# Performance work log

Measured on AMD Instinct MI355X. Metric: run time of the kernel, lower is better.

The kernel has to match this reference:

```python
import jax, jax.numpy as jnp
import numpy as np

N_NODES = 100000
N_EDGES = 3200000
IN_CH = 32
HID = 16


def setup_inputs() -> dict:
    key = jax.random.key(0)
    ks = jax.random.split(key, 8)
    x = jax.random.normal(ks[0], (N_NODES, IN_CH), dtype=jnp.float32)
    edge_index = jax.random.randint(ks[1], (2, N_EDGES), 0, N_NODES, dtype=jnp.int64)
    s1 = 1.0 / np.sqrt(IN_CH)
    s2 = 1.0 / np.sqrt(HID)
    Wl1 = jax.random.normal(ks[2], (HID, IN_CH), dtype=jnp.float32) * s1
    Wr1 = jax.random.normal(ks[3], (HID, IN_CH), dtype=jnp.float32) * s1
    b1 = jnp.zeros((HID,), dtype=jnp.float32)
    Wl2 = jax.random.normal(ks[4], (1, HID), dtype=jnp.float32) * s2
    Wr2 = jax.random.normal(ks[5], (1, HID), dtype=jnp.float32) * s2
    b2 = jnp.zeros((1,), dtype=jnp.float32)
    return {"x": x, "edge_index": edge_index, "Wl1": Wl1, "Wr1": Wr1,
            "b1": b1, "Wl2": Wl2, "Wr2": Wr2, "b2": b2}


def _sage_conv(h, src, dst, deg_inv, Wl, Wr, b):
    # mean aggregation of source features at destination nodes
    msg_sum = jax.ops.segment_sum(h[src], dst, num_segments=N_NODES)  # [N, F]
    agg = msg_sum * deg_inv[:, None]
    # lin_l(agg) + lin_r(h): lin_l carries the bias (PyG SAGEConv convention)
    return agg @ Wl.T + b + h @ Wr.T


def reference(x, edge_index, Wl1, Wr1, b1, Wl2, Wr2, b2):
    src = edge_index[0]
    dst = edge_index[1]
    deg = jax.ops.segment_sum(jnp.ones((N_EDGES,), dtype=x.dtype), dst,
                              num_segments=N_NODES)
    deg_inv = 1.0 / jnp.maximum(deg, 1.0)  # mean; nodes w/o in-edges get 0 agg

    h = _sage_conv(x, src, dst, deg_inv, Wl1, Wr1, b1)
    h = jax.nn.relu(h)
    # F.dropout in eval mode -> identity
    out = _sage_conv(h, src, dst, deg_inv, Wl2, Wr2, b2)
    return out.squeeze(-1)  # [N]
```

## Files before the change

### kernel.cpp

```cpp
#include <hip/hip_runtime.h>

#define N_NODES 100000
#define N_EDGES 3200000
#define NB_F 782
#define RSZ 4992
#define TILE 6250
#define NTILES 512
#define MAXIT 13
#define MAXB 10


__device__ __forceinline__ float bf2f_lo(unsigned int w) {
  return __uint_as_float(w << 16);
}
__device__ __forceinline__ float bf2f_hi(unsigned int w) {
  return __uint_as_float(w & 0xFFFF0000u);
}
__device__ __forceinline__ unsigned short f2bf(float f) {
  unsigned int b = __float_as_uint(f);
  return (unsigned short)((b + 0x7FFFu + ((b >> 16) & 1u)) >> 16);
}

__global__ __launch_bounds__(256) void k_init(int* __restrict__ gcur) {
  const int i = blockIdx.x * 256 + threadIdx.x;
  if (i < NB_F) gcur[i * 16] = i * RSZ;
}

__global__ __launch_bounds__(256) void k_proj1(
    const float* __restrict__ x, const float* __restrict__ Wl1,
    const float* __restrict__ Wr1, const float* __restrict__ b1,
    unsigned short* __restrict__ p1h, float* __restrict__ q1b) {
  __shared__ float sWl[16 * 32];
  __shared__ float sWr[16 * 32];
  __shared__ float sb[16];
  const int t = threadIdx.x;
  for (int i = t; i < 512; i += 256) {
    sWl[i] = Wl1[i];
    sWr[i] = Wr1[i];
  }
  if (t < 16) sb[t] = b1[t];
  __syncthreads();

  const int n = blockIdx.x * 256 + t;
  if (n >= N_NODES) return;

  float xr[32];
  const float4* xp = (const float4*)(x + (size_t)n * 32);
#pragma unroll
  for (int j = 0; j < 8; ++j) {
    float4 v = xp[j];
    xr[4 * j + 0] = v.x;
    xr[4 * j + 1] = v.y;
    xr[4 * j + 2] = v.z;
    xr[4 * j + 3] = v.w;
  }

  float pv[16], qv[16];
#pragma unroll
  for (int hh = 0; hh < 16; ++hh) {
    float a = 0.f, b = 0.f;
#pragma unroll
    for (int i = 0; i < 32; ++i) {
      a = fmaf(xr[i], sWl[hh * 32 + i], a);
      b = fmaf(xr[i], sWr[hh * 32 + i], b);
    }
    pv[hh] = a;
    qv[hh] = b + sb[hh];
  }

  unsigned int w[8];
#pragma unroll
  for (int j = 0; j < 8; ++j)
    w[j] = (unsigned int)f2bf(pv[2 * j]) |
           ((unsigned int)f2bf(pv[2 * j + 1]) << 16);
  uint4* pp = (uint4*)(p1h + (size_t)n * 16);
  pp[0] = make_uint4(w[0], w[1], w[2], w[3]);
  pp[1] = make_uint4(w[4], w[5], w[6], w[7]);

  float4* qp = (float4*)(q1b + (size_t)n * 16);
#pragma unroll
  for (int j = 0; j < 4; ++j)
    qp[j] = make_float4(qv[4 * j], qv[4 * j + 1], qv[4 * j + 2], qv[4 * j + 3]);
}

__global__ __launch_bounds__(512) void k_bscatter(const int* __restrict__ ei,
                                                  int* __restrict__ gcur,
                                                  int* __restrict__ recs) {
  __shared__ int hist[1024];
  __shared__ int rbase[NB_F];
  __shared__ int stage[TILE];
  __shared__ int seg[512];
  const int t = threadIdx.x;
  for (int i = t; i < 1024; i += 512) hist[i] = 0;
  __syncthreads();

  const int tb = blockIdx.x * TILE;
  int rec[MAXIT], aux[MAXIT];
#pragma unroll
  for (int i = 0; i < MAXIT; ++i) {
    const int pos = t + i * 512;
    if (pos < TILE) {
      const int e = tb + pos;
      const int s = ei[e];
      const int d = ei[N_EDGES + e];
      const int k = d >> 7;
      const int rank = atomicAdd(&hist[k], 1);
      rec[i] = ((d & 127) << 17) | s;
      aux[i] = (k << 16) | rank;
    } else {
      aux[i] = -1;
    }
  }
  __syncthreads();

  const int s0 = hist[2 * t], s1 = hist[2 * t + 1];
  const int my = s0 + s1;
  seg[t] = my;
  __syncthreads();
#pragma unroll
  for (int o = 1; o < 512; o <<= 1) {
    const int a = (t >= o) ? seg[t - o] : 0;
    __syncthreads();
    seg[t] += a;
    __syncthreads();
  }
  const int ex = seg[t] - my;
  hist[2 * t] = ex;
  hist[2 * t + 1] = ex + s0;
  {
    const int b = 2 * t;
    if (b + 0 < NB_F && s0) rbase[b + 0] = atomicAdd(&gcur[(b + 0) * 16], s0);
    if (b + 1 < NB_F && s1) rbase[b + 1] = atomicAdd(&gcur[(b + 1) * 16], s1);
  }
  __syncthreads();

#pragma unroll
  for (int i = 0; i < MAXIT; ++i) {
    if (aux[i] >= 0) {
      const int k = aux[i] >> 16;
      const int rank = aux[i] & 0xFFFF;
      stage[hist[k] + rank] = rec[i];
    }
  }
  __syncthreads();

  for (int pos = t; pos < TILE; pos += 512) {
    int lo = 0, hi = 1023;
    while (hi - lo > 1) {
      const int mid = (lo + hi) >> 1;
      if (hist[mid] <= pos) lo = mid;
      else hi = mid;
    }
    const int k = lo;
    const int idx = rbase[k] + (pos - hist[k]);
    if (idx < (k + 1) * RSZ) recs[idx] = stage[pos];
  }
}

__global__ __launch_bounds__(512) void k_sortagg1(
    const int* __restrict__ gcur, const int* __restrict__ recs,
    const unsigned short* __restrict__ p1h, const float* __restrict__ q1b,
    const float* __restrict__ Wl2, const float* __restrict__ Wr2,
    float* __restrict__ p2, float* __restrict__ r2,
    float* __restrict__ deg_inv) {
  __shared__ int hist[128];
  __shared__ int nstart[128];
  __shared__ int ssort[RSZ];
  __shared__ float sWl[16], sWr[16];
  const int t = threadIdx.x;
  const int kb = blockIdx.x;
  const int b0 = kb * RSZ;
  const int gend = gcur[kb * 16];
  if (t < 128) hist[t] = 0;
  if (t < 16) {
    sWl[t] = Wl2[t];
    sWr[t] = Wr2[t];
  }
  __syncthreads();

  int rc[MAXB], ax[MAXB];
#pragma unroll
  for (int i = 0; i < MAXB; ++i) {
    const int r = b0 + t + i * 512;
    if (r < gend) {
      const int rec = recs[r];
      const int local = rec >> 17;
      const int rank = atomicAdd(&hist[local], 1);
      rc[i] = rec & 0x1FFFF;
      ax[i] = (local << 13) | rank;
    } else {
      ax[i] = -1;
    }
  }
  __syncthreads();

  {
    int v = (t < 128) ? hist[t] : 0;
    if (t < 128) nstart[t] = v;
    __syncthreads();
#pragma unroll
    for (int o = 1; o < 128; o <<= 1) {
      const int a = (t < 128 && t >= o) ? nstart[t - o] : 0;
      __syncthreads();
      if (t < 128) nstart[t] += a;
      __syncthreads();
    }
    if (t < 128) nstart[t] -= v;
  }
  __syncthreads();

#pragma unroll
  for (int i = 0; i < MAXB; ++i) {
    if (ax[i] >= 0) ssort[nstart[ax[i] >> 13] + (ax[i] & 0x1FFF)] = rc[i];
  }
  __syncthreads();

  const int local = t >> 2;
  const int quad = t & 3;
  const int half = quad & 1;
  const int epar = quad >> 1;
  const int n = kb * 128 + local;
  if (n >= N_NODES) return;
  const int st = nstart[local];
  const int k = hist[local];
  const unsigned short* pb = p1h + half * 8;

  float acc[8];
#pragma unroll
  for (int i = 0; i < 8; ++i) acc[i] = 0.f;
  int j = epar;
  for (; j + 6 < k; j += 8) {
    const int s0 = ssort[st + j], s1 = ssort[st + j + 2],
              s2 = ssort[st + j + 4], s3 = ssort[st + j + 6];
    const uint4 w0 = *(const uint4*)(pb + (size_t)s0 * 16);
    const uint4 w1 = *(const uint4*)(pb + (size_t)s1 * 16);
    const uint4 w2 = *(const uint4*)(pb + (size_t)s2 * 16);
    const uint4 w3 = *(const uint4*)(pb + (size_t)s3 * 16);
    acc[0] += (bf2f_lo(w0.x) + bf2f_lo(w1.x)) + (bf2f_lo(w2.x) + bf2f_lo(w3.x));
    acc[1] += (bf2f_hi(w0.x) + bf2f_hi(w1.x)) + (bf2f_hi(w2.x) + bf2f_hi(w3.x));
    acc[2] += (bf2f_lo(w0.y) + bf2f_lo(w1.y)) + (bf2f_lo(w2.y) + bf2f_lo(w3.y));
    acc[3] += (bf2f_hi(w0.y) + bf2f_hi(w1.y)) + (bf2f_hi(w2.y) + bf2f_hi(w3.y));
    acc[4] += (bf2f_lo(w0.z) + bf2f_lo(w1.z)) + (bf2f_lo(w2.z) + bf2f_lo(w3.z));
    acc[5] += (bf2f_hi(w0.z) + bf2f_hi(w1.z)) + (bf2f_hi(w2.z) + bf2f_hi(w3.z));
    acc[6] += (bf2f_lo(w0.w) + bf2f_lo(w1.w)) + (bf2f_lo(w2.w) + bf2f_lo(w3.w));
    acc[7] += (bf2f_hi(w0.w) + bf2f_hi(w1.w)) + (bf2f_hi(w2.w) + bf2f_hi(w3.w));
  }
  for (; j < k; j += 2) {
    const uint4 w = *(const uint4*)(pb + (size_t)ssort[st + j] * 16);
    acc[0] += bf2f_lo(w.x);
    acc[1] += bf2f_hi(w.x);
    acc[2] += bf2f_lo(w.y);
    acc[3] += bf2f_hi(w.y);
    acc[4] += bf2f_lo(w.z);
    acc[5] += bf2f_hi(w.z);
    acc[6] += bf2f_lo(w.w);
    acc[7] += bf2f_hi(w.w);
  }
#pragma unroll
  for (int i = 0; i < 8; ++i) acc[i] += __shfl_xor(acc[i], 2);

  const float di = 1.f / fmaxf((float)k, 1.f);
  const float4* qp = (const float4*)(q1b + (size_t)n * 16 + half * 8);
  const float4 qa = qp[0], qb = qp[1];
  float h[8];
  h[0] = fmaxf(fmaf(acc[0], di, qa.x), 0.f);
  h[1] = fmaxf(fmaf(acc[1], di, qa.y), 0.f);
  h[2] = fmaxf(fmaf(acc[2], di, qa.z), 0.f);
  h[3] = fmaxf(fmaf(acc[3], di, qa.w), 0.f);
  h[4] = fmaxf(fmaf(acc[4], di, qb.x), 0.f);
  h[5] = fmaxf(fmaf(acc[5], di, qb.y), 0.f);
  h[6] = fmaxf(fmaf(acc[6], di, qb.z), 0.f);
  h[7] = fmaxf(fmaf(acc[7], di, qb.w), 0.f);
  float pa = 0.f, pbv = 0.f;
#pragma unroll
  for (int i = 0; i < 8; ++i) {
    pa = fmaf(h[i], sWl[half * 8 + i], pa);
    pbv = fmaf(h[i], sWr[half * 8 + i], pbv);
  }
  pa += __shfl_xor(pa, 1);
  pbv += __shfl_xor(pbv, 1);
  if (quad == 0) {
    p2[n] = pa;
    r2[n] = pbv;
    deg_inv[n] = di;
  }
}

__global__ __launch_bounds__(512) void k_agg2out(
    const int* __restrict__ gcur, const int* __restrict__ recs,
    const float* __restrict__ p2, const float* __restrict__ r2,
    const float* __restrict__ deg_inv, const float* __restrict__ b2,
    float* __restrict__ out) {
  __shared__ float u[128];
  const int t = threadIdx.x;
  const int kb = blockIdx.x;
  const int b0 = kb * RSZ;
  const int gend = gcur[kb * 16];
  if (t < 128) u[t] = 0.f;
  __syncthreads();

  int r = b0 + t;
  for (; r + 1536 < gend; r += 2048) {
    const int rec0 = recs[r];
    const int rec1 = recs[r + 512];
    const int rec2 = recs[r + 1024];
    const int rec3 = recs[r + 1536];
    const float v0 = p2[rec0 & 0x1FFFF];
    const float v1 = p2[rec1 & 0x1FFFF];
    const float v2 = p2[rec2 & 0x1FFFF];
    const float v3 = p2[rec3 & 0x1FFFF];
    atomicAdd(&u[rec0 >> 17], v0);
    atomicAdd(&u[rec1 >> 17], v1);
    atomicAdd(&u[rec2 >> 17], v2);
    atomicAdd(&u[rec3 >> 17], v3);
  }
  for (; r < gend; r += 512) {
    const int rec = recs[r];
    atomicAdd(&u[rec >> 17], p2[rec & 0x1FFFF]);
  }
  __syncthreads();
  const int n = kb * 128 + t;
  if (t < 128 && n < N_NODES)
    out[n] = fmaf(u[t], deg_inv[n], r2[n] + b2[0]);
}

extern "C" void kernel_launch(void* const* d_in, const int* in_sizes, int n_in,
                              void* d_out, int out_size, void* d_ws,
                              size_t ws_size, hipStream_t stream) {
  const float* x   = (const float*)d_in[0];
  const int*   ei  = (const int*)d_in[1];
  const float* Wl1 = (const float*)d_in[2];
  const float* Wr1 = (const float*)d_in[3];
  const float* b1  = (const float*)d_in[4];
  const float* Wl2 = (const float*)d_in[5];
  const float* Wr2 = (const float*)d_in[6];
  const float* b2  = (const float*)d_in[7];
  float* out = (float*)d_out;

  const size_t N = N_NODES;
  int* wi = (int*)d_ws;
  int* gcur = wi;
  int* recs = wi + NB_F * 16;
  unsigned short* p1h = (unsigned short*)(recs + (size_t)NB_F * RSZ);
  float* q1b     = (float*)(p1h + 16 * N);
  float* p2      = q1b + 16 * N;
  float* r2      = p2 + N;
  float* deg_inv = r2 + N;

  const int nodeBlocks = (N_NODES + 255) / 256;
  k_init<<<(NB_F + 255) / 256, 256, 0, stream>>>(gcur);
  k_proj1<<<nodeBlocks, 256, 0, stream>>>(x, Wl1, Wr1, b1, p1h, q1b);
  k_bscatter<<<NTILES, 512, 0, stream>>>(ei, gcur, recs);
  k_sortagg1<<<NB_F, 512, 0, stream>>>(gcur, recs, p1h, q1b, Wl2, Wr2, p2, r2,
                                       deg_inv);
  k_agg2out<<<NB_F, 512, 0, stream>>>(gcur, recs, p2, r2, deg_inv, b2, out);
}
```

Before: 185.7 us.

## Fuse projection with bucket scatter and reuse sorted records for layer-2 gather

Merges the node projection and the edge bucket-scatter into one launch, with block ranges picking the role, and replaces k_init with a memset that makes gcur a relative counter. The per-position binary search in the scatter becomes a per-bucket delta table held in shared memory. k_sortagg1 writes its dst-sorted source list and per-node offsets and counts back to global memory. k_agg2out can then do a per-node gather with quad reductions instead of shared-memory float atomics. This trades extra global writes in sortagg1 and a large shared-memory footprint in the fused kernel for fewer launches and less atomic contention.

```diff
diff --git a/kernel.cpp b/kernel.cpp
--- a/kernel.cpp
+++ b/kernel.cpp
@@ -6,6 +6,7 @@
 #define RSZ 4992
 #define TILE 6250
 #define NTILES 512
+#define PRJ_BLOCKS 196
 #define MAXIT 13
 #define MAXB 10
 
@@ -21,80 +22,74 @@
   return (unsigned short)((b + 0x7FFFu + ((b >> 16) & 1u)) >> 16);
 }
 
-__global__ __launch_bounds__(256) void k_init(int* __restrict__ gcur) {
-  const int i = blockIdx.x * 256 + threadIdx.x;
-  if (i < NB_F) gcur[i * 16] = i * RSZ;
-}
-
-__global__ __launch_bounds__(256) void k_proj1(
-    const float* __restrict__ x, const float* __restrict__ Wl1,
-    const float* __restrict__ Wr1, const float* __restrict__ b1,
-    unsigned short* __restrict__ p1h, float* __restrict__ q1b) {
-  __shared__ float sWl[16 * 32];
-  __shared__ float sWr[16 * 32];
-  __shared__ float sb[16];
+__global__ __launch_bounds__(512) void k_front(
+    const int* __restrict__ ei, const float* __restrict__ x,
+    const float* __restrict__ Wl1, const float* __restrict__ Wr1,
+    const float* __restrict__ b1, int* __restrict__ gcur,
+    int* __restrict__ recs, unsigned short* __restrict__ p1h,
+    float* __restrict__ q1b) {
+  __shared__ int smem[14818];
   const int t = threadIdx.x;
-  for (int i = t; i < 512; i += 256) {
-    sWl[i] = Wl1[i];
-    sWr[i] = Wr1[i];
-  }
-  if (t < 16) sb[t] = b1[t];
-  __syncthreads();
-
-  const int n = blockIdx.x * 256 + t;
-  if (n >= N_NODES) return;
-
-  float xr[32];
-  const float4* xp = (const float4*)(x + (size_t)n * 32);
-#pragma unroll
-  for (int j = 0; j < 8; ++j) {
-    float4 v = xp[j];
-    xr[4 * j + 0] = v.x;
-    xr[4 * j + 1] = v.y;
-    xr[4 * j + 2] = v.z;
-    xr[4 * j + 3] = v.w;
-  }
-
-  float pv[16], qv[16];
-#pragma unroll
-  for (int hh = 0; hh < 16; ++hh) {
-    float a = 0.f, b = 0.f;
-#pragma unroll
-    for (int i = 0; i < 32; ++i) {
-      a = fmaf(xr[i], sWl[hh * 32 + i], a);
-      b = fmaf(xr[i], sWr[hh * 32 + i], b);
-    }
-    pv[hh] = a;
-    qv[hh] = b + sb[hh];
-  }
-
-  unsigned int w[8];
-#pragma unroll
-  for (int j = 0; j < 8; ++j)
-    w[j] = (unsigned int)f2bf(pv[2 * j]) |
-           ((unsigned int)f2bf(pv[2 * j + 1]) << 16);
-  uint4* pp = (uint4*)(p1h + (size_t)n * 16);
-  pp[0] = make_uint4(w[0], w[1], w[2], w[3]);
-  pp[1] = make_uint4(w[4], w[5], w[6], w[7]);
-
-  float4* qp = (float4*)(q1b + (size_t)n * 16);
-#pragma unroll
-  for (int j = 0; j < 4; ++j)
-    qp[j] = make_float4(qv[4 * j], qv[4 * j + 1], qv[4 * j + 2], qv[4 * j + 3]);
-}
-
-__global__ __launch_bounds__(512) void k_bscatter(const int* __restrict__ ei,
-                                                  int* __restrict__ gcur,
-                                                  int* __restrict__ recs) {
-  __shared__ int hist[1024];
-  __shared__ int rbase[NB_F];
-  __shared__ int stage[TILE];
-  __shared__ int seg[512];
-  const int t = threadIdx.x;
+
+  if (blockIdx.x < PRJ_BLOCKS) {
+    float* sWl = (float*)smem;
+    float* sWr = (float*)smem + 512;
+    float* sb  = (float*)smem + 1024;
+    sWl[t] = Wl1[t];
+    sWr[t] = Wr1[t];
+    if (t < 16) sb[t] = b1[t];
+    __syncthreads();
+
+    const int n = blockIdx.x * 512 + t;
+    if (n >= N_NODES) return;
+
+    float xr[32];
+    const float4* xp = (const float4*)(x + (size_t)n * 32);
+#pragma unroll
+    for (int j = 0; j < 8; ++j) {
+      float4 v = xp[j];
+      xr[4 * j + 0] = v.x;
+      xr[4 * j + 1] = v.y;
+      xr[4 * j + 2] = v.z;
+      xr[4 * j + 3] = v.w;
+    }
+    float pv[16], qv[16];
+#pragma unroll
+    for (int hh = 0; hh < 16; ++hh) {
+      float a = 0.f, b = 0.f;
+#pragma unroll
+      for (int i = 0; i < 32; ++i) {
+        a = fmaf(xr[i], sWl[hh * 32 + i], a);
+        b = fmaf(xr[i], sWr[hh * 32 + i], b);
+      }
+      pv[hh] = a;
+      qv[hh] = b + sb[hh];
+    }
+    unsigned int w[8];
+#pragma unroll
+    for (int j = 0; j < 8; ++j)
+      w[j] = (unsigned int)f2bf(pv[2 * j]) |
+             ((unsigned int)f2bf(pv[2 * j + 1]) << 16);
+    uint4* pp = (uint4*)(p1h + (size_t)n * 16);
+    pp[0] = make_uint4(w[0], w[1], w[2], w[3]);
+    pp[1] = make_uint4(w[4], w[5], w[6], w[7]);
+    float4* qp = (float4*)(q1b + (size_t)n * 16);
+#pragma unroll
+    for (int j = 0; j < 4; ++j)
+      qp[j] =
+          make_float4(qv[4 * j], qv[4 * j + 1], qv[4 * j + 2], qv[4 * j + 3]);
+    return;
+  }
+
+  int* hist  = smem;
+  int* rbase = smem + 1024;
+  int* seg   = smem + 1806;
+  int* stage = smem + 2318;
+  int* dlt   = smem + 8568;
   for (int i = t; i < 1024; i += 512) hist[i] = 0;
   __syncthreads();
 
-  const int tb = blockIdx.x * TILE;
+  const int tb = (blockIdx.x - PRJ_BLOCKS) * TILE;
   int rec[MAXIT], aux[MAXIT];
 #pragma unroll
   for (int i = 0; i < MAXIT; ++i) {
@@ -129,8 +124,9 @@
   hist[2 * t + 1] = ex + s0;
   {
     const int b = 2 * t;
-    if (b + 0 < NB_F && s0) rbase[b + 0] = atomicAdd(&gcur[(b + 0) * 16], s0);
-    if (b + 1 < NB_F && s1) rbase[b + 1] = atomicAdd(&gcur[(b + 1) * 16], s1);
+    if (b < NB_F && s0) rbase[b] = b * RSZ + atomicAdd(&gcur[b * 16], s0);
+    if (b + 1 < NB_F && s1)
+      rbase[b + 1] = (b + 1) * RSZ + atomicAdd(&gcur[(b + 1) * 16], s1);
   }
   __syncthreads();
 
@@ -142,27 +138,29 @@
       stage[hist[k] + rank] = rec[i];
     }
   }
+  for (int k2 = t; k2 < NB_F; k2 += 512) {
+    const int st = hist[k2];
+    const int en = hist[k2 + 1];
+    if (en > st) {
+      const int dv = rbase[k2] - st;
+      for (int p = st; p < en; ++p) dlt[p] = dv;
+    }
+  }
   __syncthreads();
 
   for (int pos = t; pos < TILE; pos += 512) {
-    int lo = 0, hi = 1023;
-    while (hi - lo > 1) {
-      const int mid = (lo + hi) >> 1;
-      if (hist[mid] <= pos) lo = mid;
-      else hi = mid;
-    }
-    const int k = lo;
-    const int idx = rbase[k] + (pos - hist[k]);
-    if (idx < (k + 1) * RSZ) recs[idx] = stage[pos];
+    const int idx = dlt[pos] + pos;
+    if ((unsigned)idx < (unsigned)(NB_F * RSZ)) recs[idx] = stage[pos];
   }
 }
 
 __global__ __launch_bounds__(512) void k_sortagg1(
-    const int* __restrict__ gcur, const int* __restrict__ recs,
+    const int* __restrict__ gcur, int* __restrict__ recs,
     const unsigned short* __restrict__ p1h, const float* __restrict__ q1b,
     const float* __restrict__ Wl2, const float* __restrict__ Wr2,
     float* __restrict__ p2, float* __restrict__ r2,
-    float* __restrict__ deg_inv) {
+    float* __restrict__ deg_inv, int* __restrict__ node_off,
+    int* __restrict__ node_cnt) {
   __shared__ int hist[128];
   __shared__ int nstart[128];
   __shared__ int ssort[RSZ];
@@ -170,7 +168,7 @@
   const int t = threadIdx.x;
   const int kb = blockIdx.x;
   const int b0 = kb * RSZ;
-  const int gend = gcur[kb * 16];
+  const int gend = b0 + gcur[kb * 16];
   if (t < 128) hist[t] = 0;
   if (t < 16) {
     sWl[t] = Wl2[t];
@@ -214,6 +212,13 @@
     if (ax[i] >= 0) ssort[nstart[ax[i] >> 13] + (ax[i] & 0x1FFF)] = rc[i];
   }
   __syncthreads();
+
+  const int T = gend - b0;
+  for (int j2 = t; j2 < T; j2 += 512) recs[b0 + j2] = ssort[j2];
+  if (t < 128) {
+    node_off[kb * 128 + t] = b0 + nstart[t];
+    node_cnt[kb * 128 + t] = hist[t];
+  }
 
   const int local = t >> 2;
   const int quad = t & 3;
@@ -287,41 +292,25 @@
 }
 
 __global__ __launch_bounds__(512) void k_agg2out(
-    const int* __restrict__ gcur, const int* __restrict__ recs,
-    const float* __restrict__ p2, const float* __restrict__ r2,
-    const float* __restrict__ deg_inv, const float* __restrict__ b2,
-    float* __restrict__ out) {
-  __shared__ float u[128];
+    const int* __restrict__ node_off, const int* __restrict__ node_cnt,
+    const int* __restrict__ recs, const float* __restrict__ p2,
+    const float* __restrict__ r2, const float* __restrict__ deg_inv,
+    const float* __restrict__ b2, float* __restrict__ out) {
   const int t = threadIdx.x;
-  const int kb = blockIdx.x;
-  const int b0 = kb * RSZ;
-  const int gend = gcur[kb * 16];
-  if (t < 128) u[t] = 0.f;
-  __syncthreads();
-
-  int r = b0 + t;
-  for (; r + 1536 < gend; r += 2048) {
-    const int rec0 = recs[r];
-    const int rec1 = recs[r + 512];
-    const int rec2 = recs[r + 1024];
-    const int rec3 = recs[r + 1536];
-    const float v0 = p2[rec0 & 0x1FFFF];
-    const float v1 = p2[rec1 & 0x1FFFF];
-    const float v2 = p2[rec2 & 0x1FFFF];
-    const float v3 = p2[rec3 & 0x1FFFF];
-    atomicAdd(&u[rec0 >> 17], v0);
-    atomicAdd(&u[rec1 >> 17], v1);
-    atomicAdd(&u[rec2 >> 17], v2);
-    atomicAdd(&u[rec3 >> 17], v3);
-  }
-  for (; r < gend; r += 512) {
-    const int rec = recs[r];
-    atomicAdd(&u[rec >> 17], p2[rec & 0x1FFFF]);
-  }
-  __syncthreads();
-  const int n = kb * 128 + t;
-  if (t < 128 && n < N_NODES)
-    out[n] = fmaf(u[t], deg_inv[n], r2[n] + b2[0]);
+  const int n = blockIdx.x * 128 + (t >> 2);
+  const int c = t & 3;
+  if (n >= N_NODES) return;
+  const int k0 = node_off[n];
+  const int k = node_cnt[n];
+  const int* sl = recs + k0;
+
+  float u = 0.f;
+  int j = c;
+  for (; j + 4 < k; j += 8) u += p2[sl[j]] + p2[sl[j + 4]];
+  for (; j < k; j += 4) u += p2[sl[j]];
+  u += __shfl_xor(u, 1);
+  u += __shfl_xor(u, 2);
+  if (c == 0) out[n] = fmaf(u, deg_inv[n], r2[n] + b2[0]);
 }
 
 extern "C" void kernel_launch(void* const* d_in, const int* in_sizes, int n_in,
@@ -339,19 +328,21 @@
 
   const size_t N = N_NODES;
   int* wi = (int*)d_ws;
-  int* gcur = wi;
-  int* recs = wi + NB_F * 16;
+  int* gcur     = wi;
+  int* node_off = wi + NB_F * 16;
+  int* node_cnt = node_off + NB_F * 128;
+  int* recs     = node_cnt + NB_F * 128;
   unsigned short* p1h = (unsigned short*)(recs + (size_t)NB_F * RSZ);
   float* q1b     = (float*)(p1h + 16 * N);
   float* p2      = q1b + 16 * N;
   float* r2      = p2 + N;
   float* deg_inv = r2 + N;
 
-  const int nodeBlocks = (N_NODES + 255) / 256;
-  k_init<<<(NB_F + 255) / 256, 256, 0, stream>>>(gcur);
-  k_proj1<<<nodeBlocks, 256, 0, stream>>>(x, Wl1, Wr1, b1, p1h, q1b);
-  k_bscatter<<<NTILES, 512, 0, stream>>>(ei, gcur, recs);
+  hipMemsetAsync(gcur, 0, NB_F * 16 * sizeof(int), stream);
+  k_front<<<PRJ_BLOCKS + NTILES, 512, 0, stream>>>(ei, x, Wl1, Wr1, b1, gcur,
+                                                   recs, p1h, q1b);
   k_sortagg1<<<NB_F, 512, 0, stream>>>(gcur, recs, p1h, q1b, Wl2, Wr2, p2, r2,
-                                       deg_inv);
-  k_agg2out<<<NB_F, 512, 0, stream>>>(gcur, recs, p2, r2, deg_inv, b2, out);
-}
+                                       deg_inv, node_off, node_cnt);
+  k_agg2out<<<NB_F, 512, 0, stream>>>(node_off, node_cnt, recs, p2, r2,
+                                      deg_inv, b2, out);
+}
```

Result: faster. 176.2 us (-5.1%).
